# Kernel tuning notes

Hardware: AMD Instinct MI355X
Metric: run time of the kernel (lower is better)

Reference implementation:

```python
import jax, jax.numpy as jnp
import numpy as np

H = 1024      # hidden_size
NH = 16       # num_heads
HD = H // NH  # head_dim
MLP_DIM = 4096
EPS = 1e-6


def setup_inputs() -> dict:
    key = jax.random.key(0)
    ks = jax.random.split(key, 16)
    B, S = 8, 1024
    s_in = 1.0 / np.sqrt(H)
    s_mlp = 1.0 / np.sqrt(MLP_DIM)
    return {
        "x": jax.random.normal(ks[0], (B, S, H), jnp.float32),
        "ln1_g": jnp.ones((H,), jnp.float32),
        "ln1_b": jnp.zeros((H,), jnp.float32),
        "Wq": jax.random.normal(ks[1], (H, H), jnp.float32) * s_in,
        "bq": jnp.zeros((H,), jnp.float32),
        "Wk": jax.random.normal(ks[2], (H, H), jnp.float32) * s_in,
        "bk": jnp.zeros((H,), jnp.float32),
        "Wv": jax.random.normal(ks[3], (H, H), jnp.float32) * s_in,
        "bv": jnp.zeros((H,), jnp.float32),
        "Wo": jax.random.normal(ks[4], (H, H), jnp.float32) * s_in,
        "bo": jnp.zeros((H,), jnp.float32),
        "ln2_g": jnp.ones((H,), jnp.float32),
        "ln2_b": jnp.zeros((H,), jnp.float32),
        "W1": jax.random.normal(ks[5], (H, MLP_DIM), jnp.float32) * s_in,
        "b1": jnp.zeros((MLP_DIM,), jnp.float32),
        "W2": jax.random.normal(ks[6], (MLP_DIM, H), jnp.float32) * s_mlp,
        "b2": jnp.zeros((H,), jnp.float32),
    }


def _layernorm(x, g, b):
    mu = jnp.mean(x, axis=-1, keepdims=True)
    var = jnp.mean(jnp.square(x - mu), axis=-1, keepdims=True)
    return (x - mu) * jax.lax.rsqrt(var + EPS) * g + b


def reference(x, ln1_g, ln1_b, Wq, bq, Wk, bk, Wv, bv, Wo, bo,
              ln2_g, ln2_b, W1, b1, W2, b2):
    B, S, _ = x.shape
    # pre-LN attention
    h = _layernorm(x, ln1_g, ln1_b)
    q = (h @ Wq + bq).reshape(B, S, NH, HD).transpose(0, 2, 1, 3)  # bhsd
    k = (h @ Wk + bk).reshape(B, S, NH, HD).transpose(0, 2, 1, 3)
    v = (h @ Wv + bv).reshape(B, S, NH, HD).transpose(0, 2, 1, 3)
    scale = HD ** -0.5
    scores = jnp.einsum('bhqd,bhkd->bhqk', q, k) * scale
    weights = jax.nn.softmax(scores, axis=-1)
    attended = jnp.einsum('bhqk,bhkd->bhqd', weights, v)
    attended = attended.transpose(0, 2, 1, 3).reshape(B, S, H)
    x = x + attended @ Wo + bo
    # pre-LN MLP
    h = _layernorm(x, ln2_g, ln2_b)
    h = jax.nn.gelu(h @ W1 + b1, approximate=False)
    x = x + h @ W2 + b2
    return x
```

## Files before the change

kernel.cpp:

```cpp
#include <hip/hip_runtime.h>

#define H_DIM 1024
#define NHEADS 16
#define HD 64
#define SEQ 1024
#define BATCH 8
#define ROWS (BATCH*SEQ)
#define MLPD 4096

typedef __bf16 bf16x8 __attribute__((ext_vector_type(8)));
typedef float f32x4 __attribute__((ext_vector_type(4)));

__device__ __forceinline__ unsigned short f2bf(float f) {
    unsigned u = __float_as_uint(f);
    unsigned r = u + 0x7FFFu + ((u >> 16) & 1u);
    return (unsigned short)(r >> 16);
}

__global__ void transpose_w(const float* __restrict__ in, unsigned short* __restrict__ out,
                            int K, int N)
{
    __shared__ float tile[32][33];
    const int n0 = blockIdx.x * 32, k0 = blockIdx.y * 32;
    const int tx = threadIdx.x, ty = threadIdx.y;
    #pragma unroll
    for (int i = ty; i < 32; i += 8)
        tile[i][tx] = in[(size_t)(k0 + i) * N + n0 + tx];
    __syncthreads();
    #pragma unroll
    for (int i = ty; i < 32; i += 8)
        out[(size_t)(n0 + i) * K + k0 + tx] = f2bf(tile[tx][i]);
}

__global__ void transpose_v(const unsigned short* __restrict__ in,
                            unsigned short* __restrict__ out)
{
    __shared__ unsigned short tile[32][33];
    const size_t base = (size_t)blockIdx.z * (SEQ * HD);
    const int d0 = blockIdx.x * 32, s0 = blockIdx.y * 32;
    const int tx = threadIdx.x, ty = threadIdx.y;
    #pragma unroll
    for (int i = ty; i < 32; i += 8)
        tile[i][tx] = in[base + (size_t)(s0 + i) * HD + d0 + tx];
    __syncthreads();
    const int fx = ((tx & 12) << 1) | ((tx & 16) >> 2) | (tx & 3);
    #pragma unroll
    for (int i = ty; i < 32; i += 8)
        out[base + (size_t)(d0 + i) * SEQ + s0 + fx] = tile[tx][i];
}

__global__ __launch_bounds__(256) void ln_kernel(const float* __restrict__ x,
    const float* __restrict__ g, const float* __restrict__ b,
    unsigned short* __restrict__ out)
{
    __shared__ float red[4];
    const int row = blockIdx.x;
    const int tid = threadIdx.x;
    const float4 v = *(const float4*)(x + (size_t)row * H_DIM + tid * 4);
    float s = v.x + v.y + v.z + v.w;
    #pragma unroll
    for (int off = 32; off >= 1; off >>= 1) s += __shfl_xor(s, off);
    if ((tid & 63) == 0) red[tid >> 6] = s;
    __syncthreads();
    const float mu = (red[0] + red[1] + red[2] + red[3]) * (1.0f / H_DIM);
    __syncthreads();
    const float dx = v.x - mu, dy = v.y - mu, dz = v.z - mu, dw = v.w - mu;
    float q = dx * dx + dy * dy + dz * dz + dw * dw;
    #pragma unroll
    for (int off = 32; off >= 1; off >>= 1) q += __shfl_xor(q, off);
    if ((tid & 63) == 0) red[tid >> 6] = q;
    __syncthreads();
    const float var = (red[0] + red[1] + red[2] + red[3]) * (1.0f / H_DIM);
    const float rstd = rsqrtf(var + 1e-6f);
    const float4 gv = *(const float4*)(g + tid * 4);
    const float4 bv = *(const float4*)(b + tid * 4);
    ushort4 o;
    o.x = f2bf(dx * rstd * gv.x + bv.x);
    o.y = f2bf(dy * rstd * gv.y + bv.y);
    o.z = f2bf(dz * rstd * gv.z + bv.z);
    o.w = f2bf(dw * rstd * gv.w + bv.w);
    *(ushort4*)(out + (size_t)row * H_DIM + tid * 4) = o;
}

template<int MODE>
__global__ __launch_bounds__(256) void gemm_dp(
    const unsigned short* __restrict__ A, const unsigned short* __restrict__ Bt,
    const float* __restrict__ bias0, const float* __restrict__ bias1,
    const float* __restrict__ bias2, const float* resid,
    float* outF, unsigned short* __restrict__ outH,
    int N, int K, int gn)
{
    __shared__ __align__(16) unsigned short As[128 * 64];
    __shared__ __align__(16) unsigned short Bs[128 * 64];

    const int tid = threadIdx.x, lane = tid & 63;
    const int w = tid >> 6;
    const int wm = w >> 1, wn = w & 1;

    const int nwg = gridDim.x;
    const int swzb = (blockIdx.x & 7) * (nwg >> 3) + (blockIdx.x >> 3);
    const int bm = swzb / gn, bn = swzb % gn;

    const int srow = tid >> 3;
    const int sc = (tid & 7) ^ (srow & 7);
    const unsigned short* Abase = A  + (size_t)(bm * 128) * K;
    const unsigned short* Bbase = Bt + (size_t)(bn * 128) * K;

    auto stage = [&](int kt) {
        const size_t kofs = (size_t)kt * 64 + sc * 8;
        #pragma unroll
        for (int q = 0; q < 4; ++q)
            __builtin_amdgcn_global_load_lds(
                (__attribute__((address_space(1))) void*)(Abase + (size_t)(q * 32 + srow) * K + kofs),
                (__attribute__((address_space(3))) void*)(&As[q * 2048 + tid * 8]), 16, 0, 0);
        #pragma unroll
        for (int q = 0; q < 4; ++q)
            __builtin_amdgcn_global_load_lds(
                (__attribute__((address_space(1))) void*)(Bbase + (size_t)(q * 32 + srow) * K + kofs),
                (__attribute__((address_space(3))) void*)(&Bs[q * 2048 + tid * 8]), 16, 0, 0);
    };

    const int lr = lane & 15, hk = lane >> 4;
    const int px0 = (hk ^ (lr & 7)) * 8;
    const int px1 = px0 ^ 32;
    const int arow = (wm * 64 + lr) * 64;
    const int brow = (wn * 64 + lr) * 64;

    f32x4 acc[4][4] = {};
    const int nkt = K >> 6;

    for (int t = 0; t < nkt; ++t) {
        stage(t);
        __syncthreads();

        const unsigned short* Ab = &As[arow];
        const unsigned short* Bb = &Bs[brow];

        bf16x8 a0[4], b0[4], a1[4], b1[4];
        #pragma unroll
        for (int i = 0; i < 4; ++i) { b0[i] = *(const bf16x8*)(Bb + i * 1024 + px0);
                                      a0[i] = *(const bf16x8*)(Ab + i * 1024 + px0); }
        #pragma unroll
        for (int i = 0; i < 4; ++i) { b1[i] = *(const bf16x8*)(Bb + i * 1024 + px1);
                                      a1[i] = *(const bf16x8*)(Ab + i * 1024 + px1); }
        __builtin_amdgcn_s_setprio(1);
        #pragma unroll
        for (int mi = 0; mi < 4; ++mi)
            #pragma unroll
            for (int ni = 0; ni < 4; ++ni)
                acc[mi][ni] = __builtin_amdgcn_mfma_f32_16x16x32_bf16(a0[mi], b0[ni], acc[mi][ni], 0, 0, 0);
        __builtin_amdgcn_s_setprio(0);
        __builtin_amdgcn_s_setprio(1);
        #pragma unroll
        for (int mi = 0; mi < 4; ++mi)
            #pragma unroll
            for (int ni = 0; ni < 4; ++ni)
                acc[mi][ni] = __builtin_amdgcn_mfma_f32_16x16x32_bf16(a1[mi], b1[ni], acc[mi][ni], 0, 0, 0);
        __builtin_amdgcn_s_setprio(0);
        __syncthreads();
    }

    #pragma unroll
    for (int mi = 0; mi < 4; ++mi) {
        #pragma unroll
        for (int ni = 0; ni < 4; ++ni) {
            const int gcol = bn * 128 + wn * 64 + ni * 16 + lr;
            #pragma unroll
            for (int r = 0; r < 4; ++r) {
                const int grow = bm * 128 + wm * 64 + mi * 16 + hk * 4 + r;
                if (MODE == 0) {
                    const int which = gcol >> 10;
                    const int col = gcol & 1023;
                    const float* bp = (which == 0) ? bias0 : (which == 1) ? bias1 : bias2;
                    const float v = acc[mi][ni][r] + bp[col];
                    const int b_ = grow >> 10, s_ = grow & 1023, h_ = col >> 6, d_ = col & 63;
                    outH[(size_t)which * (ROWS * 1024) +
                         (size_t)(b_ * NHEADS + h_) * 65536 + s_ * 64 + d_] = f2bf(v);
                } else if (MODE == 2) {
                    const float v = acc[mi][ni][r] + bias0[gcol];
                    const size_t idx = (size_t)grow * N + gcol;
                    outF[idx] = resid[idx] + v;
                } else {
                    const float v = acc[mi][ni][r] + bias0[gcol];
                    const float t3 = fmaf(0.044715f * v * v, v, v);
                    const float e  = __builtin_amdgcn_exp2f(-2.3022086f * t3);
                    const float ge = v * __builtin_amdgcn_rcpf(1.0f + e);
                    outH[(size_t)grow * N + gcol] = f2bf(ge);
                }
            }
        }
    }
}

__global__ __launch_bounds__(512) void gemm8k(
    const unsigned short* __restrict__ A, const unsigned short* __restrict__ Bt,
    const float* __restrict__ bias, unsigned short* __restrict__ outH,
    int N, int K, int gn)
{
    __shared__ __align__(16) unsigned short As[2][2][8192];
    __shared__ __align__(16) unsigned short Bs[2][2][8192];

    const int tid = threadIdx.x, lane = tid & 63;
    const int w = tid >> 6;
    const int wm = w >> 2, wn = w & 3;

    const int nwg = gridDim.x;
    const int swzb = (blockIdx.x & 7) * (nwg >> 3) + (blockIdx.x >> 3);
    const int bm = swzb / gn, bn = swzb % gn;

    const unsigned short* Abase = A  + (size_t)(bm * 256) * K;
    const unsigned short* Bbase = Bt + (size_t)(bn * 256) * K;

    int srow[2], soff[2];
    #pragma unroll
    for (int j = 0; j < 2; ++j) {
        const int slot = j * 512 + tid;
        srow[j] = slot >> 2;
        const int p = slot & 3;
        soff[j] = (p ^ ((srow[j] >> 1) & 3)) * 8;
    }

    auto stageKH = [&](int buf, int kt, int s) {
        #pragma unroll
        for (int j = 0; j < 2; ++j) {
            const size_t off = (size_t)srow[j] * K + (size_t)kt * 64 + s * 32 + soff[j];
            __builtin_amdgcn_global_load_lds(
                (__attribute__((address_space(1))) void*)(Abase + off),
                (__attribute__((address_space(3))) void*)(&As[buf][s][(j * 512 + tid) * 8]), 16, 0, 0);
            __builtin_amdgcn_global_load_lds(
                (__attribute__((address_space(1))) void*)(Bbase + off),
                (__attribute__((address_space(3))) void*)(&Bs[buf][s][(j * 512 + tid) * 8]), 16, 0, 0);
        }
    };

    const int lr = lane & 15, hk = lane >> 4;
    int aoff[8], boff[4];
    #pragma unroll
    for (int mf = 0; mf < 8; ++mf) {
        const int R = wm * 128 + mf * 16 + lr;
        aoff[mf] = R * 32 + ((hk ^ ((R >> 1) & 3)) * 8);
    }
    #pragma unroll
    for (int nf = 0; nf < 4; ++nf) {
        const int R = wn * 64 + nf * 16 + lr;
        boff[nf] = R * 32 + ((hk ^ ((R >> 1) & 3)) * 8);
    }

    f32x4 acc[8][4] = {};
    const int nkt = K >> 6;

    stageKH(0, 0, 0);
    stageKH(0, 0, 1);
    asm volatile("s_waitcnt vmcnt(4)" ::: "memory");
    __builtin_amdgcn_s_barrier();
    asm volatile("" ::: "memory");

    for (int t = 0; t < nkt; ++t) {
        const int buf = t & 1;
        #pragma unroll
        for (int s = 0; s < 2; ++s) {
            const unsigned short* Ar = &As[buf][s][0];
            const unsigned short* Br = &Bs[buf][s][0];
            bf16x8 af[8], bf[4];
            #pragma unroll
            for (int nf = 0; nf < 4; ++nf) bf[nf] = *(const bf16x8*)(Br + boff[nf]);
            #pragma unroll
            for (int mf = 0; mf < 8; ++mf) af[mf] = *(const bf16x8*)(Ar + aoff[mf]);

            if (t + 1 < nkt) {
                stageKH(buf ^ 1, t + 1, s);
                asm volatile("s_waitcnt vmcnt(4)" ::: "memory");
            } else {
                asm volatile("s_waitcnt vmcnt(0)" ::: "memory");
            }
            __builtin_amdgcn_s_barrier();
            asm volatile("" ::: "memory");

            __builtin_amdgcn_s_setprio(1);
            #pragma unroll
            for (int mf = 0; mf < 8; ++mf)
                #pragma unroll
                for (int nf = 0; nf < 4; ++nf)
                    acc[mf][nf] = __builtin_amdgcn_mfma_f32_16x16x32_bf16(af[mf], bf[nf], acc[mf][nf], 0, 0, 0);
            __builtin_amdgcn_s_setprio(0);
        }
    }

    #pragma unroll
    for (int mf = 0; mf < 8; ++mf) {
        #pragma unroll
        for (int nf = 0; nf < 4; ++nf) {
            const int gcol = bn * 256 + wn * 64 + nf * 16 + lr;
            #pragma unroll
            for (int r = 0; r < 4; ++r) {
                const int grow = bm * 256 + wm * 128 + mf * 16 + hk * 4 + r;
                const float v = acc[mf][nf][r] + bias[gcol];
                const float t3 = fmaf(0.044715f * v * v, v, v);
                const float e  = __builtin_amdgcn_exp2f(-2.3022086f * t3);
                const float ge = v * __builtin_amdgcn_rcpf(1.0f + e);
                outH[(size_t)grow * N + gcol] = f2bf(ge);
            }
        }
    }
}

__global__ __launch_bounds__(256) void attn_kernel(const unsigned short* __restrict__ q,
    const unsigned short* __restrict__ k, const unsigned short* __restrict__ vT,
    unsigned short* __restrict__ out)
{
    __shared__ __align__(16) unsigned short Ks[2][4096];
    __shared__ __align__(16) unsigned short Vs[2][4096];
    const int tid = threadIdx.x, lane = tid & 63, w = tid >> 6;
    const int bh = blockIdx.y;
    const int q0 = blockIdx.x * 64;
    const size_t headBase = (size_t)bh * (SEQ * HD);

    const int qrow = q0 + w * 16 + (lane & 15);
    const unsigned short* qp = q + headBase + (size_t)qrow * HD + (lane >> 4) * 8;
    const bf16x8 qf0 = *(const bf16x8*)(qp);
    const bf16x8 qf1 = *(const bf16x8*)(qp + 32);

    float lacc = 0.f;
    f32x4 oacc[4] = {};

    const int srow = tid >> 3;
    const int swz  = ((tid & 7) ^ (srow & 7)) * 8;
    const int pc   = (lane >> 4) ^ (lane & 7);

    auto stage = [&](int buf, int kt) {
        #pragma unroll
        for (int s = 0; s < 2; ++s) {
            const unsigned short* gk = k  + headBase + (size_t)(kt + s * 32 + srow) * HD + swz;
            const unsigned short* gv = vT + headBase + (size_t)(s * 32 + srow) * SEQ + kt + swz;
            __builtin_amdgcn_global_load_lds((__attribute__((address_space(1))) void*)gk,
                (__attribute__((address_space(3))) void*)(&Ks[buf][s * 2048 + w * 512]), 16, 0, 0);
            __builtin_amdgcn_global_load_lds((__attribute__((address_space(1))) void*)gv,
                (__attribute__((address_space(3))) void*)(&Vs[buf][s * 2048 + w * 512]), 16, 0, 0);
        }
    };

    stage(0, 0);
    __syncthreads();

    const float C1 = 0.125f * 1.44269504f;
    const float C2 = -4.0f * 1.44269504f;

    for (int t = 0; t < 16; ++t) {
        const int cur = t & 1;
        if (t < 15) stage(cur ^ 1, (t + 1) * 64);

        const unsigned short* KB = &Ks[cur][0];
        const unsigned short* VB = &Vs[cur][0];

        f32x4 s4[4] = {};
        #pragma unroll
        for (int ni = 0; ni < 4; ++ni) {
            const unsigned short* pk = KB + (ni * 16 + (lane & 15)) * 64;
            s4[ni] = __builtin_amdgcn_mfma_f32_16x16x32_bf16(*(const bf16x8*)(pk + pc * 8),       qf0, s4[ni], 0, 0, 0);
            s4[ni] = __builtin_amdgcn_mfma_f32_16x16x32_bf16(*(const bf16x8*)(pk + (pc ^ 4) * 8), qf1, s4[ni], 0, 0, 0);
        }

        unsigned U[4][2];
        float ls = 0.f;
        #pragma unroll
        for (int ni = 0; ni < 4; ++ni) {
            const float p0 = __builtin_amdgcn_exp2f(fmaf(s4[ni][0], C1, C2));
            const float p1 = __builtin_amdgcn_exp2f(fmaf(s4[ni][1], C1, C2));
            const float p2 = __builtin_amdgcn_exp2f(fmaf(s4[ni][2], C1, C2));
            const float p3 = __builtin_amdgcn_exp2f(fmaf(s4[ni][3], C1, C2));
            ls += (p0 + p1) + (p2 + p3);
            asm("v_cvt_pk_bf16_f32 %0, %1, %2" : "=v"(U[ni][0]) : "v"(p0), "v"(p1));
            asm("v_cvt_pk_bf16_f32 %0, %1, %2" : "=v"(U[ni][1]) : "v"(p2), "v"(p3));
        }
        lacc += ls;

        union { unsigned u[4]; bf16x8 v; } W0, W1;
        W0.u[0] = U[0][0]; W0.u[1] = U[0][1]; W0.u[2] = U[1][0]; W0.u[3] = U[1][1];
        W1.u[0] = U[2][0]; W1.u[1] = U[2][1]; W1.u[2] = U[3][0]; W1.u[3] = U[3][1];

        #pragma unroll
        for (int nd = 0; nd < 4; ++nd) {
            const unsigned short* pv = VB + (nd * 16 + (lane & 15)) * 64;
            oacc[nd] = __builtin_amdgcn_mfma_f32_16x16x32_bf16(*(const bf16x8*)(pv + pc * 8),       W0.v, oacc[nd], 0, 0, 0);
            oacc[nd] = __builtin_amdgcn_mfma_f32_16x16x32_bf16(*(const bf16x8*)(pv + (pc ^ 4) * 8), W1.v, oacc[nd], 0, 0, 0);
        }

        __syncthreads();
    }

    float l = lacc;
    l += __shfl_xor(l, 16);
    l += __shfl_xor(l, 32);
    const float inv = 1.0f / l;

    const int b_ = bh >> 4, h_ = bh & 15;
    const int s_ = q0 + w * 16 + (lane & 15);
    const int hh = (lane >> 4) * 4;
    #pragma unroll
    for (int nd = 0; nd < 4; ++nd) {
        ushort4 o;
        o.x = f2bf(oacc[nd][0] * inv);
        o.y = f2bf(oacc[nd][1] * inv);
        o.z = f2bf(oacc[nd][2] * inv);
        o.w = f2bf(oacc[nd][3] * inv);
        *(ushort4*)(out + (size_t)(b_ * SEQ + s_) * H_DIM + h_ * 64 + nd * 16 + hh) = o;
    }
}

extern "C" void kernel_launch(void* const* d_in, const int* in_sizes, int n_in,
                              void* d_out, int out_size, void* d_ws, size_t ws_size,
                              hipStream_t stream)
{
    const float* x    = (const float*)d_in[0];
    const float* ln1g = (const float*)d_in[1];
    const float* ln1b = (const float*)d_in[2];
    const float* Wq   = (const float*)d_in[3];
    const float* bq   = (const float*)d_in[4];
    const float* Wk   = (const float*)d_in[5];
    const float* bk   = (const float*)d_in[6];
    const float* Wv   = (const float*)d_in[7];
    const float* bv   = (const float*)d_in[8];
    const float* Wo   = (const float*)d_in[9];
    const float* bo   = (const float*)d_in[10];
    const float* ln2g = (const float*)d_in[11];
    const float* ln2b = (const float*)d_in[12];
    const float* W1   = (const float*)d_in[13];
    const float* b1   = (const float*)d_in[14];
    const float* W2   = (const float*)d_in[15];
    const float* b2   = (const float*)d_in[16];
    float* out = (float*)d_out;

    char* ws = (char*)d_ws;
    const size_t MB = 1024 * 1024;
    unsigned short* h1  = (unsigned short*)(ws);
    unsigned short* qb  = (unsigned short*)(ws + 16 * MB);
    unsigned short* kb  = (unsigned short*)(ws + 32 * MB);
    unsigned short* vb  = (unsigned short*)(ws + 48 * MB);
    unsigned short* vTb = (unsigned short*)(ws + 64 * MB);
    unsigned short* mlp = (unsigned short*)(ws + 16 * MB);
    unsigned short* ao  = h1;
    unsigned short* WqT = (unsigned short*)(ws + 80 * MB);
    unsigned short* WkT = (unsigned short*)(ws + 82 * MB);
    unsigned short* WvT = (unsigned short*)(ws + 84 * MB);
    unsigned short* WoT = (unsigned short*)(ws + 86 * MB);
    unsigned short* W1T = (unsigned short*)(ws + 88 * MB);
    unsigned short* W2T = (unsigned short*)(ws + 96 * MB);

    const dim3 tb(32, 8);
    transpose_w<<<dim3(32, 32),  tb, 0, stream>>>(Wq, WqT, 1024, 1024);
    transpose_w<<<dim3(32, 32),  tb, 0, stream>>>(Wk, WkT, 1024, 1024);
    transpose_w<<<dim3(32, 32),  tb, 0, stream>>>(Wv, WvT, 1024, 1024);
    transpose_w<<<dim3(32, 32),  tb, 0, stream>>>(Wo, WoT, 1024, 1024);
    transpose_w<<<dim3(128, 32), tb, 0, stream>>>(W1, W1T, 1024, 4096);
    transpose_w<<<dim3(32, 128), tb, 0, stream>>>(W2, W2T, 4096, 1024);

    ln_kernel<<<ROWS, 256, 0, stream>>>(x, ln1g, ln1b, h1);

    gemm_dp<0><<<1536, 256, 0, stream>>>(h1, WqT, bq, bk, bv, nullptr, nullptr, qb, 3072, 1024, 24);

    transpose_v<<<dim3(2, 32, 128), tb, 0, stream>>>(vb, vTb);

    attn_kernel<<<dim3(16, 128), 256, 0, stream>>>(qb, kb, vTb, ao);

    gemm_dp<2><<<512, 256, 0, stream>>>(ao, WoT, bo, bo, bo, x, out, nullptr, 1024, 1024, 8);

    ln_kernel<<<ROWS, 256, 0, stream>>>(out, ln2g, ln2b, h1);

    gemm8k<<<512, 512, 0, stream>>>(h1, W1T, b1, mlp, 4096, 1024, 16);
    gemm_dp<2><<<512, 256, 0, stream>>>(mlp, W2T, b2, b2, b2, out, out, nullptr, 1024, 4096, 8);
}
```

Measured before the change: 362.7 us.

## Merge weight transposes, templatize big GEMM, double query rows per attention block

The six weight-transpose launches become one combined kernel that picks the matrix from the block index, which removes per-launch overhead. The gemm8k kernel becomes a templated gemm_kp that supports other N tile widths, though only the 256-wide GELU variant is launched. Each attention wave now handles two 16-row query groups, so a block covers 128 queries and every K/V tile loaded into LDS is reused twice. This halves the attention grid and raises register use per thread.

```diff
diff --git a/kernel.cpp b/kernel.cpp
--- a/kernel.cpp
+++ b/kernel.cpp
@@ -17,11 +17,28 @@
     return (unsigned short)(r >> 16);
 }
 
-__global__ void transpose_w(const float* __restrict__ in, unsigned short* __restrict__ out,
-                            int K, int N)
+__global__ void transpose_all(const float* __restrict__ Wq, const float* __restrict__ Wk,
+                              const float* __restrict__ Wv, const float* __restrict__ Wo,
+                              const float* __restrict__ W1, const float* __restrict__ W2,
+                              unsigned short* __restrict__ WqT, unsigned short* __restrict__ WkT,
+                              unsigned short* __restrict__ WvT, unsigned short* __restrict__ WoT,
+                              unsigned short* __restrict__ W1T, unsigned short* __restrict__ W2T)
 {
     __shared__ float tile[32][33];
-    const int n0 = blockIdx.x * 32, k0 = blockIdx.y * 32;
+    const int id = blockIdx.x;
+    const float* in; unsigned short* outp; int K, N, t;
+    if (id < 4096) {
+        const int wsel = id >> 10; t = id & 1023;
+        in   = (wsel == 0) ? Wq  : (wsel == 1) ? Wk  : (wsel == 2) ? Wv  : Wo;
+        outp = (wsel == 0) ? WqT : (wsel == 1) ? WkT : (wsel == 2) ? WvT : WoT;
+        K = 1024; N = 1024;
+    } else if (id < 8192) {
+        t = id - 4096; in = W1; outp = W1T; K = 1024; N = 4096;
+    } else {
+        t = id - 8192; in = W2; outp = W2T; K = 4096; N = 1024;
+    }
+    const int ntx = N >> 5;
+    const int n0 = (t % ntx) * 32, k0 = (t / ntx) * 32;
     const int tx = threadIdx.x, ty = threadIdx.y;
     #pragma unroll
     for (int i = ty; i < 32; i += 8)
@@ -29,7 +46,7 @@
     __syncthreads();
     #pragma unroll
     for (int i = ty; i < 32; i += 8)
-        out[(size_t)(n0 + i) * K + k0 + tx] = f2bf(tile[tx][i]);
+        outp[(size_t)(n0 + i) * K + k0 + tx] = f2bf(tile[tx][i]);
 }
 
 __global__ void transpose_v(const unsigned short* __restrict__ in,
@@ -180,8 +197,139 @@
                     const float v = acc[mi][ni][r] + bias0[gcol];
                     const size_t idx = (size_t)grow * N + gcol;
                     outF[idx] = resid[idx] + v;
+                }
+            }
+        }
+    }
+}
+
+template<int MODE, int BN>
+__global__ __launch_bounds__(512) void gemm_kp(
+    const unsigned short* __restrict__ A, const unsigned short* __restrict__ Bt,
+    const float* __restrict__ bias0, const float* __restrict__ bias1,
+    const float* __restrict__ bias2, const float* resid,
+    float* outF, unsigned short* __restrict__ outH,
+    int N, int K, int gn)
+{
+    constexpr int WN = (BN == 256) ? 4 : 2;
+    constexpr int WM = 8 / WN;
+    constexpr int RM = 256 / WM;
+    constexpr int RN = BN / WN;
+    constexpr int MR = RM / 16;
+    constexpr int NR = RN / 16;
+    constexpr int BJ = BN / 128;
+
+    __shared__ __align__(16) unsigned short As[2][2][8192];
+    __shared__ __align__(16) unsigned short Bs[2][2][BN * 32];
+
+    const int tid = threadIdx.x, lane = tid & 63;
+    const int w = tid >> 6;
+    const int wm = w / WN, wn = w % WN;
+
+    const int nwg = gridDim.x;
+    const int swzb = (blockIdx.x & 7) * (nwg >> 3) + (blockIdx.x >> 3);
+    const int bm = swzb / gn, bn = swzb % gn;
+
+    const unsigned short* Abase = A  + (size_t)(bm * 256) * K;
+    const unsigned short* Bbase = Bt + (size_t)(bn * BN) * K;
+
+    int asrow[2], asoff[2];
+    #pragma unroll
+    for (int j = 0; j < 2; ++j) {
+        const int slot = j * 512 + tid;
+        asrow[j] = slot >> 2;
+        asoff[j] = ((slot & 3) ^ ((asrow[j] >> 1) & 3)) * 8;
+    }
+    int bsrow[BJ], bsoff[BJ];
+    #pragma unroll
+    for (int j = 0; j < BJ; ++j) {
+        const int slot = j * 512 + tid;
+        bsrow[j] = slot >> 2;
+        bsoff[j] = ((slot & 3) ^ ((bsrow[j] >> 1) & 3)) * 8;
+    }
+
+    auto stageKH = [&](int buf, int kt, int s) {
+        #pragma unroll
+        for (int j = 0; j < 2; ++j)
+            __builtin_amdgcn_global_load_lds(
+                (__attribute__((address_space(1))) void*)(Abase + (size_t)asrow[j] * K + (size_t)kt * 64 + s * 32 + asoff[j]),
+                (__attribute__((address_space(3))) void*)(&As[buf][s][(j * 512 + tid) * 8]), 16, 0, 0);
+        #pragma unroll
+        for (int j = 0; j < BJ; ++j)
+            __builtin_amdgcn_global_load_lds(
+                (__attribute__((address_space(1))) void*)(Bbase + (size_t)bsrow[j] * K + (size_t)kt * 64 + s * 32 + bsoff[j]),
+                (__attribute__((address_space(3))) void*)(&Bs[buf][s][(j * 512 + tid) * 8]), 16, 0, 0);
+    };
+
+    const int lr = lane & 15, hk = lane >> 4;
+    int aoff[MR], boff[NR];
+    #pragma unroll
+    for (int mf = 0; mf < MR; ++mf) {
+        const int R = wm * RM + mf * 16 + lr;
+        aoff[mf] = R * 32 + ((hk ^ ((R >> 1) & 3)) * 8);
+    }
+    #pragma unroll
+    for (int nf = 0; nf < NR; ++nf) {
+        const int R = wn * RN + nf * 16 + lr;
+        boff[nf] = R * 32 + ((hk ^ ((R >> 1) & 3)) * 8);
+    }
+
+    f32x4 acc[MR][NR] = {};
+    const int nkt = K >> 6;
+
+    stageKH(0, 0, 0);
+    stageKH(0, 0, 1);
+    if constexpr (BJ == 2) asm volatile("s_waitcnt vmcnt(4)" ::: "memory");
+    else                   asm volatile("s_waitcnt vmcnt(3)" ::: "memory");
+    __builtin_amdgcn_s_barrier();
+    asm volatile("" ::: "memory");
+
+    for (int t = 0; t < nkt; ++t) {
+        const int buf = t & 1;
+        #pragma unroll
+        for (int s = 0; s < 2; ++s) {
+            const unsigned short* Ar = &As[buf][s][0];
+            const unsigned short* Br = &Bs[buf][s][0];
+            bf16x8 af[MR], bf[NR];
+            #pragma unroll
+            for (int nf = 0; nf < NR; ++nf) bf[nf] = *(const bf16x8*)(Br + boff[nf]);
+            #pragma unroll
+            for (int mf = 0; mf < MR; ++mf) af[mf] = *(const bf16x8*)(Ar + aoff[mf]);
+
+            if (t + 1 < nkt) {
+                stageKH(buf ^ 1, t + 1, s);
+                if constexpr (BJ == 2) asm volatile("s_waitcnt vmcnt(4)" ::: "memory");
+                else                   asm volatile("s_waitcnt vmcnt(3)" ::: "memory");
+            } else {
+                asm volatile("s_waitcnt vmcnt(0)" ::: "memory");
+            }
+            __builtin_amdgcn_s_barrier();
+            asm volatile("" ::: "memory");
+
+            __builtin_amdgcn_s_setprio(1);
+            #pragma unroll
+            for (int mf = 0; mf < MR; ++mf)
+                #pragma unroll
+                for (int nf = 0; nf < NR; ++nf)
+                    acc[mf][nf] = __builtin_amdgcn_mfma_f32_16x16x32_bf16(af[mf], bf[nf], acc[mf][nf], 0, 0, 0);
+            __builtin_amdgcn_s_setprio(0);
+        }
+    }
+
+    #pragma unroll
+    for (int mf = 0; mf < MR; ++mf) {
+        #pragma unroll
+        for (int nf = 0; nf < NR; ++nf) {
+            const int gcol = bn * BN + wn * RN + nf * 16 + lr;
+            #pragma unroll
+            for (int r = 0; r < 4; ++r) {
+                const int grow = bm * 256 + wm * RM + mf * 16 + hk * 4 + r;
+                if (MODE == 2) {
+                    const float v = acc[mf][nf][r] + bias0[gcol];
+                    const size_t idx = (size_t)grow * N + gcol;
+                    outF[idx] = resid[idx] + v;
                 } else {
-                    const float v = acc[mi][ni][r] + bias0[gcol];
+                    const float v = acc[mf][nf][r] + bias0[gcol];
                     const float t3 = fmaf(0.044715f * v * v, v, v);
                     const float e  = __builtin_amdgcn_exp2f(-2.3022086f * t3);
                     const float ge = v * __builtin_amdgcn_rcpf(1.0f + e);
@@ -192,118 +340,6 @@
     }
 }
 
-__global__ __launch_bounds__(512) void gemm8k(
-    const unsigned short* __restrict__ A, const unsigned short* __restrict__ Bt,
-    const float* __restrict__ bias, unsigned short* __restrict__ outH,
-    int N, int K, int gn)
-{
-    __shared__ __align__(16) unsigned short As[2][2][8192];
-    __shared__ __align__(16) unsigned short Bs[2][2][8192];
-
-    const int tid = threadIdx.x, lane = tid & 63;
-    const int w = tid >> 6;
-    const int wm = w >> 2, wn = w & 3;
-
-    const int nwg = gridDim.x;
-    const int swzb = (blockIdx.x & 7) * (nwg >> 3) + (blockIdx.x >> 3);
-    const int bm = swzb / gn, bn = swzb % gn;
-
-    const unsigned short* Abase = A  + (size_t)(bm * 256) * K;
-    const unsigned short* Bbase = Bt + (size_t)(bn * 256) * K;
-
-    int srow[2], soff[2];
-    #pragma unroll
-    for (int j = 0; j < 2; ++j) {
-        const int slot = j * 512 + tid;
-        srow[j] = slot >> 2;
-        const int p = slot & 3;
-        soff[j] = (p ^ ((srow[j] >> 1) & 3)) * 8;
-    }
-
-    auto stageKH = [&](int buf, int kt, int s) {
-        #pragma unroll
-        for (int j = 0; j < 2; ++j) {
-            const size_t off = (size_t)srow[j] * K + (size_t)kt * 64 + s * 32 + soff[j];
-            __builtin_amdgcn_global_load_lds(
-                (__attribute__((address_space(1))) void*)(Abase + off),
-                (__attribute__((address_space(3))) void*)(&As[buf][s][(j * 512 + tid) * 8]), 16, 0, 0);
-            __builtin_amdgcn_global_load_lds(
-                (__attribute__((address_space(1))) void*)(Bbase + off),
-                (__attribute__((address_space(3))) void*)(&Bs[buf][s][(j * 512 + tid) * 8]), 16, 0, 0);
-        }
-    };
-
-    const int lr = lane & 15, hk = lane >> 4;
-    int aoff[8], boff[4];
-    #pragma unroll
-    for (int mf = 0; mf < 8; ++mf) {
-        const int R = wm * 128 + mf * 16 + lr;
-        aoff[mf] = R * 32 + ((hk ^ ((R >> 1) & 3)) * 8);
-    }
-    #pragma unroll
-    for (int nf = 0; nf < 4; ++nf) {
-        const int R = wn * 64 + nf * 16 + lr;
-        boff[nf] = R * 32 + ((hk ^ ((R >> 1) & 3)) * 8);
-    }
-
-    f32x4 acc[8][4] = {};
-    const int nkt = K >> 6;
-
-    stageKH(0, 0, 0);
-    stageKH(0, 0, 1);
-    asm volatile("s_waitcnt vmcnt(4)" ::: "memory");
-    __builtin_amdgcn_s_barrier();
-    asm volatile("" ::: "memory");
-
-    for (int t = 0; t < nkt; ++t) {
-        const int buf = t & 1;
-        #pragma unroll
-        for (int s = 0; s < 2; ++s) {
-            const unsigned short* Ar = &As[buf][s][0];
-            const unsigned short* Br = &Bs[buf][s][0];
-            bf16x8 af[8], bf[4];
-            #pragma unroll
-            for (int nf = 0; nf < 4; ++nf) bf[nf] = *(const bf16x8*)(Br + boff[nf]);
-            #pragma unroll
-            for (int mf = 0; mf < 8; ++mf) af[mf] = *(const bf16x8*)(Ar + aoff[mf]);
-
-            if (t + 1 < nkt) {
-                stageKH(buf ^ 1, t + 1, s);
-                asm volatile("s_waitcnt vmcnt(4)" ::: "memory");
-            } else {
-                asm volatile("s_waitcnt vmcnt(0)" ::: "memory");
-            }
-            __builtin_amdgcn_s_barrier();
-            asm volatile("" ::: "memory");
-
-            __builtin_amdgcn_s_setprio(1);
-            #pragma unroll
-            for (int mf = 0; mf < 8; ++mf)
-                #pragma unroll
-                for (int nf = 0; nf < 4; ++nf)
-                    acc[mf][nf] = __builtin_amdgcn_mfma_f32_16x16x32_bf16(af[mf], bf[nf], acc[mf][nf], 0, 0, 0);
-            __builtin_amdgcn_s_setprio(0);
-        }
-    }
-
-    #pragma unroll
-    for (int mf = 0; mf < 8; ++mf) {
-        #pragma unroll
-        for (int nf = 0; nf < 4; ++nf) {
-            const int gcol = bn * 256 + wn * 64 + nf * 16 + lr;
-            #pragma unroll
-            for (int r = 0; r < 4; ++r) {
-                const int grow = bm * 256 + wm * 128 + mf * 16 + hk * 4 + r;
-                const float v = acc[mf][nf][r] + bias[gcol];
-                const float t3 = fmaf(0.044715f * v * v, v, v);
-                const float e  = __builtin_amdgcn_exp2f(-2.3022086f * t3);
-                const float ge = v * __builtin_amdgcn_rcpf(1.0f + e);
-                outH[(size_t)grow * N + gcol] = f2bf(ge);
-            }
-        }
-    }
-}
-
 __global__ __launch_bounds__(256) void attn_kernel(const unsigned short* __restrict__ q,
     const unsigned short* __restrict__ k, const unsigned short* __restrict__ vT,
     unsigned short* __restrict__ out)
@@ -312,16 +348,21 @@
     __shared__ __align__(16) unsigned short Vs[2][4096];
     const int tid = threadIdx.x, lane = tid & 63, w = tid >> 6;
     const int bh = blockIdx.y;
-    const int q0 = blockIdx.x * 64;
+    const int q0 = blockIdx.x * 128;
     const size_t headBase = (size_t)bh * (SEQ * HD);
 
-    const int qrow = q0 + w * 16 + (lane & 15);
-    const unsigned short* qp = q + headBase + (size_t)qrow * HD + (lane >> 4) * 8;
-    const bf16x8 qf0 = *(const bf16x8*)(qp);
-    const bf16x8 qf1 = *(const bf16x8*)(qp + 32);
-
-    float lacc = 0.f;
-    f32x4 oacc[4] = {};
+    const int qr = lane & 15;
+    bf16x8 qf[2][2];
+    #pragma unroll
+    for (int g = 0; g < 2; ++g) {
+        const unsigned short* qp = q + headBase
+            + (size_t)(q0 + w * 32 + g * 16 + qr) * HD + (lane >> 4) * 8;
+        qf[g][0] = *(const bf16x8*)(qp);
+        qf[g][1] = *(const bf16x8*)(qp + 32);
+    }
+
+    float lacc[2] = {0.f, 0.f};
+    f32x4 oacc[2][4] = {};
 
     const int srow = tid >> 3;
     const int swz  = ((tid & 7) ^ (srow & 7)) * 8;
@@ -352,58 +393,63 @@
         const unsigned short* KB = &Ks[cur][0];
         const unsigned short* VB = &Vs[cur][0];
 
-        f32x4 s4[4] = {};
-        #pragma unroll
-        for (int ni = 0; ni < 4; ++ni) {
-            const unsigned short* pk = KB + (ni * 16 + (lane & 15)) * 64;
-            s4[ni] = __builtin_amdgcn_mfma_f32_16x16x32_bf16(*(const bf16x8*)(pk + pc * 8),       qf0, s4[ni], 0, 0, 0);
-            s4[ni] = __builtin_amdgcn_mfma_f32_16x16x32_bf16(*(const bf16x8*)(pk + (pc ^ 4) * 8), qf1, s4[ni], 0, 0, 0);
+        #pragma unroll
+        for (int g = 0; g < 2; ++g) {
+            f32x4 s4[4] = {};
+            #pragma unroll
+            for (int ni = 0; ni < 4; ++ni) {
+                const unsigned short* pk = KB + (ni * 16 + qr) * 64;
+                s4[ni] = __builtin_amdgcn_mfma_f32_16x16x32_bf16(*(const bf16x8*)(pk + pc * 8),       qf[g][0], s4[ni], 0, 0, 0);
+                s4[ni] = __builtin_amdgcn_mfma_f32_16x16x32_bf16(*(const bf16x8*)(pk + (pc ^ 4) * 8), qf[g][1], s4[ni], 0, 0, 0);
+            }
+
+            unsigned U[4][2];
+            float ls = 0.f;
+            #pragma unroll
+            for (int ni = 0; ni < 4; ++ni) {
+                const float p0 = __builtin_amdgcn_exp2f(fmaf(s4[ni][0], C1, C2));
+                const float p1 = __builtin_amdgcn_exp2f(fmaf(s4[ni][1], C1, C2));
+                const float p2 = __builtin_amdgcn_exp2f(fmaf(s4[ni][2], C1, C2));
+                const float p3 = __builtin_amdgcn_exp2f(fmaf(s4[ni][3], C1, C2));
+                ls += (p0 + p1) + (p2 + p3);
+                asm("v_cvt_pk_bf16_f32 %0, %1, %2" : "=v"(U[ni][0]) : "v"(p0), "v"(p1));
+                asm("v_cvt_pk_bf16_f32 %0, %1, %2" : "=v"(U[ni][1]) : "v"(p2), "v"(p3));
+            }
+            lacc[g] += ls;
+
+            union { unsigned u[4]; bf16x8 v; } W0, W1;
+            W0.u[0] = U[0][0]; W0.u[1] = U[0][1]; W0.u[2] = U[1][0]; W0.u[3] = U[1][1];
+            W1.u[0] = U[2][0]; W1.u[1] = U[2][1]; W1.u[2] = U[3][0]; W1.u[3] = U[3][1];
+
+            #pragma unroll
+            for (int nd = 0; nd < 4; ++nd) {
+                const unsigned short* pv = VB + (nd * 16 + qr) * 64;
+                oacc[g][nd] = __builtin_amdgcn_mfma_f32_16x16x32_bf16(*(const bf16x8*)(pv + pc * 8),       W0.v, oacc[g][nd], 0, 0, 0);
+                oacc[g][nd] = __builtin_amdgcn_mfma_f32_16x16x32_bf16(*(const bf16x8*)(pv + (pc ^ 4) * 8), W1.v, oacc[g][nd], 0, 0, 0);
+            }
         }
 
-        unsigned U[4][2];
-        float ls = 0.f;
-        #pragma unroll
-        for (int ni = 0; ni < 4; ++ni) {
-            const float p0 = __builtin_amdgcn_exp2f(fmaf(s4[ni][0], C1, C2));
-            const float p1 = __builtin_amdgcn_exp2f(fmaf(s4[ni][1], C1, C2));
-            const float p2 = __builtin_amdgcn_exp2f(fmaf(s4[ni][2], C1, C2));
-            const float p3 = __builtin_amdgcn_exp2f(fmaf(s4[ni][3], C1, C2));
-            ls += (p0 + p1) + (p2 + p3);
-            asm("v_cvt_pk_bf16_f32 %0, %1, %2" : "=v"(U[ni][0]) : "v"(p0), "v"(p1));
-            asm("v_cvt_pk_bf16_f32 %0, %1, %2" : "=v"(U[ni][1]) : "v"(p2), "v"(p3));
+        __syncthreads();
+    }
+
+    const int b_ = bh >> 4, h_ = bh & 15;
+    const int hh = (lane >> 4) * 4;
+    #pragma unroll
+    for (int g = 0; g < 2; ++g) {
+        float l = lacc[g];
+        l += __shfl_xor(l, 16);
+        l += __shfl_xor(l, 32);
+        const float inv = 1.0f / l;
+        const int s_ = q0 + w * 32 + g * 16 + qr;
+        #pragma unroll
+        for (int nd = 0; nd < 4; ++nd) {
+            ushort4 o;
+            o.x = f2bf(oacc[g][nd][0] * inv);
+            o.y = f2bf(oacc[g][nd][1] * inv);
+            o.z = f2bf(oacc[g][nd][2] * inv);
+            o.w = f2bf(oacc[g][nd][3] * inv);
+            *(ushort4*)(out + (size_t)(b_ * SEQ + s_) * H_DIM + h_ * 64 + nd * 16 + hh) = o;
         }
-        lacc += ls;
-
-        union { unsigned u[4]; bf16x8 v; } W0, W1;
-        W0.u[0] = U[0][0]; W0.u[1] = U[0][1]; W0.u[2] = U[1][0]; W0.u[3] = U[1][1];
-        W1.u[0] = U[2][0]; W1.u[1] = U[2][1]; W1.u[2] = U[3][0]; W1.u[3] = U[3][1];
-
-        #pragma unroll
-        for (int nd = 0; nd < 4; ++nd) {
-            const unsigned short* pv = VB + (nd * 16 + (lane & 15)) * 64;
-            oacc[nd] = __builtin_amdgcn_mfma_f32_16x16x32_bf16(*(const bf16x8*)(pv + pc * 8),       W0.v, oacc[nd], 0, 0, 0);
-            oacc[nd] = __builtin_amdgcn_mfma_f32_16x16x32_bf16(*(const bf16x8*)(pv + (pc ^ 4) * 8), W1.v, oacc[nd], 0, 0, 0);
-        }
-
-        __syncthreads();
-    }
-
-    float l = lacc;
-    l += __shfl_xor(l, 16);
-    l += __shfl_xor(l, 32);
-    const float inv = 1.0f / l;
-
-    const int b_ = bh >> 4, h_ = bh & 15;
-    const int s_ = q0 + w * 16 + (lane & 15);
-    const int hh = (lane >> 4) * 4;
-    #pragma unroll
-    for (int nd = 0; nd < 4; ++nd) {
-        ushort4 o;
-        o.x = f2bf(oacc[nd][0] * inv);
-        o.y = f2bf(oacc[nd][1] * inv);
-        o.z = f2bf(oacc[nd][2] * inv);
-        o.w = f2bf(oacc[nd][3] * inv);
-        *(ushort4*)(out + (size_t)(b_ * SEQ + s_) * H_DIM + h_ * 64 + nd * 16 + hh) = o;
     }
 }
 
@@ -446,26 +492,21 @@
     unsigned short* W1T = (unsigned short*)(ws + 88 * MB);
     unsigned short* W2T = (unsigned short*)(ws + 96 * MB);
 
-    const dim3 tb(32, 8);
-    transpose_w<<<dim3(32, 32),  tb, 0, stream>>>(Wq, WqT, 1024, 1024);
-    transpose_w<<<dim3(32, 32),  tb, 0, stream>>>(Wk, WkT, 1024, 1024);
-    transpose_w<<<dim3(32, 32),  tb, 0, stream>>>(Wv, WvT, 1024, 1024);
-    transpose_w<<<dim3(32, 32),  tb, 0, stream>>>(Wo, WoT, 1024, 1024);
-    transpose_w<<<dim3(128, 32), tb, 0, stream>>>(W1, W1T, 1024, 4096);
-    transpose_w<<<dim3(32, 128), tb, 0, stream>>>(W2, W2T, 4096, 1024);
+    transpose_all<<<12288, dim3(32, 8), 0, stream>>>(Wq, Wk, Wv, Wo, W1, W2,
+                                                     WqT, WkT, WvT, WoT, W1T, W2T);
 
     ln_kernel<<<ROWS, 256, 0, stream>>>(x, ln1g, ln1b, h1);
 
     gemm_dp<0><<<1536, 256, 0, stream>>>(h1, WqT, bq, bk, bv, nullptr, nullptr, qb, 3072, 1024, 24);
 
-    transpose_v<<<dim3(2, 32, 128), tb, 0, stream>>>(vb, vTb);
-
-    attn_kernel<<<dim3(16, 128), 256, 0, stream>>>(qb, kb, vTb, ao);
+    transpose_v<<<dim3(2, 32, 128), dim3(32, 8), 0, stream>>>(vb, vTb);
+
+    attn_kernel<<<dim3(8, 128), 256, 0, stream>>>(qb, kb, vTb, ao);
 
     gemm_dp<2><<<512, 256, 0, stream>>>(ao, WoT, bo, bo, bo, x, out, nullptr, 1024, 1024, 8);
 
     ln_kernel<<<ROWS, 256, 0, stream>>>(out, ln2g, ln2b, h1);
 
-    gemm8k<<<512, 512, 0, stream>>>(h1, W1T, b1, mlp, 4096, 1024, 16);
+    gemm_kp<3, 256><<<512, 512, 0, stream>>>(h1, W1T, b1, b1, b1, nullptr, nullptr, mlp, 4096, 1024, 16);
     gemm_dp<2><<<512, 256, 0, stream>>>(mlp, W2T, b2, b2, b2, out, out, nullptr, 1024, 4096, 8);
 }
```

Result: faster. 352.2 us (-2.9%).
